# Optimization experiments

Hardware: AMD Instinct MI355X
Metric: run time of the kernel (lower is better)

The kernel has to match this reference:

```python
import jax, jax.numpy as jnp
import numpy as np

B = 65536
STATE_DIM = 96
ACTION_DIM = 32
IN_FEATURES = STATE_DIM + ACTION_DIM  # 128
HIDDEN = 256
NUM_HEADS = 200
OUT_FEATURES = 1


def setup_inputs() -> dict:
    key = jax.random.key(0)
    ks = jax.random.split(key, 9)
    state = jax.random.normal(ks[0], (B, STATE_DIM), dtype=jnp.float32)
    action = jax.random.normal(ks[1], (B, ACTION_DIM), dtype=jnp.float32)
    alphas = jax.random.uniform(ks[2], (NUM_HEADS,), dtype=jnp.float32)
    W1 = jax.random.normal(ks[3], (HIDDEN, IN_FEATURES), dtype=jnp.float32) * 0.05
    b1 = jax.random.normal(ks[4], (HIDDEN,), dtype=jnp.float32) * 0.05
    W2 = jax.random.normal(ks[5], (HIDDEN, HIDDEN), dtype=jnp.float32) * 0.05
    b2 = jax.random.normal(ks[6], (HIDDEN,), dtype=jnp.float32) * 0.05
    # stacked head params: heads[h] is Linear(256 -> out_features)
    Wh = jax.random.normal(ks[7], (NUM_HEADS, OUT_FEATURES, HIDDEN), dtype=jnp.float32) * 0.05
    bh = jax.random.normal(ks[8], (NUM_HEADS, OUT_FEATURES), dtype=jnp.float32) * 0.05
    return {"state": state, "action": action, "alphas": alphas,
            "W1": W1, "b1": b1, "W2": W2, "b2": b2, "Wh": Wh, "bh": bh}


def reference(state, action, alphas, W1, b1, W2, b2, Wh, bh):
    x = jnp.concatenate([state, action], axis=1)          # [B, 128]
    x = jax.nn.relu(x @ W1.T + b1)                         # [B, 256]
    x = jax.nn.relu(x @ W2.T + b2)                         # [B, 256]
    # sum_h alpha_h * (x @ Wh[h].T + bh[h])  ==  x @ (sum_h alpha_h Wh[h]).T + sum_h alpha_h bh[h]
    Wc = jnp.einsum('h,hod->od', alphas, Wh)               # [out, 256]
    bc = jnp.einsum('h,ho->o', alphas, bh)                 # [out]
    return x @ Wc.T + bc                                   # [B, out]
```

## Files before the change

kernel.cpp:

```cpp
#include <hip/hip_runtime.h>
#include <hip/hip_bf16.h>


#define B_TOTAL 65536
#define SDIM 96
#define ADIM 32
#define IN_F 128
#define HID 256
#define NHEADS 200
#define BM 64
#define H1_PITCH 260

typedef __bf16 bf16;
typedef __attribute__((ext_vector_type(8))) __bf16 bf16x8;
typedef __attribute__((ext_vector_type(4))) float f32x4;

__global__ void prep_kernel(const float* __restrict__ W1, const float* __restrict__ W2,
                            const float* __restrict__ alphas, const float* __restrict__ Wh,
                            const float* __restrict__ bh,
                            bf16* __restrict__ W1bf, bf16* __restrict__ W2bf,
                            float* __restrict__ Wc) {
    int tid = blockIdx.x * blockDim.x + threadIdx.x;
    if (tid < IN_F * HID) W1bf[tid] = (bf16)W1[tid];
    if (tid < HID * HID)  W2bf[tid] = (bf16)W2[tid];
    if (tid < HID) {
        float acc = 0.f;
        #pragma unroll 8
        for (int h = 0; h < NHEADS; ++h) acc += alphas[h] * Wh[h * HID + tid];
        Wc[tid] = acc;
    }
    if (tid == HID) {
        float acc = 0.f;
        for (int h = 0; h < NHEADS; ++h) acc += alphas[h] * bh[h];
        Wc[HID] = acc;
    }
}

__global__ __launch_bounds__(256, 4) void critic_kernel(
        const float* __restrict__ state, const float* __restrict__ action,
        const float* __restrict__ b1, const float* __restrict__ b2,
        const bf16* __restrict__ W1bf, const bf16* __restrict__ W2bf,
        const float* __restrict__ Wc, float* __restrict__ out) {

    __shared__ bf16 h1s[BM * H1_PITCH];
    __shared__ float sWc[HID];
    __shared__ float sPart[4][BM];

    const int tid  = threadIdx.x;
    const int wave = tid >> 6;
    const int lane = tid & 63;
    const int q    = lane >> 4;
    const int ln   = lane & 15;
    const int colw = wave * 64;
    const int row0 = blockIdx.x * BM;

    sWc[tid] = Wc[tid];

    f32x4 acc[4][4];
    #pragma unroll
    for (int mt = 0; mt < 4; ++mt)
        #pragma unroll
        for (int nt = 0; nt < 4; ++nt)
            acc[mt][nt] = (f32x4){0.f, 0.f, 0.f, 0.f};

    #pragma unroll
    for (int ks = 0; ks < 4; ++ks) {
        const int k0 = ks * 32 + q * 8;
        bf16x8 a[4], b[4];
        #pragma unroll
        for (int mt = 0; mt < 4; ++mt) {
            const size_t row = row0 + mt * 16 + ln;
            const float* src = (ks < 3) ? (state  + row * SDIM + k0)
                                        : (action + row * ADIM + q * 8);
            float4 v0 = ((const float4*)src)[0];
            float4 v1 = ((const float4*)src)[1];
            a[mt] = (bf16x8){(bf16)v0.x, (bf16)v0.y, (bf16)v0.z, (bf16)v0.w,
                             (bf16)v1.x, (bf16)v1.y, (bf16)v1.z, (bf16)v1.w};
        }
        #pragma unroll
        for (int nt = 0; nt < 4; ++nt)
            b[nt] = *(const bf16x8*)&W1bf[(size_t)(colw + nt * 16 + ln) * IN_F + k0];
        #pragma unroll
        for (int mt = 0; mt < 4; ++mt)
            #pragma unroll
            for (int nt = 0; nt < 4; ++nt)
                acc[mt][nt] = __builtin_amdgcn_mfma_f32_16x16x32_bf16(a[mt], b[nt], acc[mt][nt], 0, 0, 0);
    }

    #pragma unroll
    for (int nt = 0; nt < 4; ++nt) {
        const int n      = colw + nt * 16 + ln;
        const float bias = b1[n];
        #pragma unroll
        for (int mt = 0; mt < 4; ++mt)
            #pragma unroll
            for (int r = 0; r < 4; ++r) {
                float v = acc[mt][nt][r] + bias;
                v = v > 0.f ? v : 0.f;
                h1s[(mt * 16 + q * 4 + r) * H1_PITCH + n] = (bf16)v;
            }
    }
    __syncthreads();

    #pragma unroll
    for (int mt = 0; mt < 4; ++mt)
        #pragma unroll
        for (int nt = 0; nt < 4; ++nt)
            acc[mt][nt] = (f32x4){0.f, 0.f, 0.f, 0.f};

    #pragma unroll
    for (int ks = 0; ks < 8; ++ks) {
        const int k0 = ks * 32 + q * 8;
        bf16x8 a[4], b[4];
        #pragma unroll
        for (int mt = 0; mt < 4; ++mt)
            a[mt] = *(const bf16x8*)&h1s[(mt * 16 + ln) * H1_PITCH + k0];
        #pragma unroll
        for (int nt = 0; nt < 4; ++nt)
            b[nt] = *(const bf16x8*)&W2bf[(size_t)(colw + nt * 16 + ln) * HID + k0];
        #pragma unroll
        for (int mt = 0; mt < 4; ++mt)
            #pragma unroll
            for (int nt = 0; nt < 4; ++nt)
                acc[mt][nt] = __builtin_amdgcn_mfma_f32_16x16x32_bf16(a[mt], b[nt], acc[mt][nt], 0, 0, 0);
    }

    float partial[4][4];
    #pragma unroll
    for (int mt = 0; mt < 4; ++mt)
        #pragma unroll
        for (int r = 0; r < 4; ++r)
            partial[mt][r] = 0.f;

    #pragma unroll
    for (int nt = 0; nt < 4; ++nt) {
        const int n      = colw + nt * 16 + ln;
        const float bias = b2[n];
        const float wc   = sWc[n];
        #pragma unroll
        for (int mt = 0; mt < 4; ++mt)
            #pragma unroll
            for (int r = 0; r < 4; ++r) {
                float v = acc[mt][nt][r] + bias;
                v = v > 0.f ? v : 0.f;
                partial[mt][r] += v * wc;
            }
    }

    #pragma unroll
    for (int off = 1; off < 16; off <<= 1)
        #pragma unroll
        for (int mt = 0; mt < 4; ++mt)
            #pragma unroll
            for (int r = 0; r < 4; ++r)
                partial[mt][r] += __shfl_xor(partial[mt][r], off, 64);

    if (ln == 0) {
        #pragma unroll
        for (int mt = 0; mt < 4; ++mt)
            #pragma unroll
            for (int r = 0; r < 4; ++r)
                sPart[wave][mt * 16 + q * 4 + r] = partial[mt][r];
    }
    __syncthreads();

    if (tid < BM) {
        float v = sPart[0][tid] + sPart[1][tid] + sPart[2][tid] + sPart[3][tid] + Wc[HID];
        out[row0 + tid] = v;
    }
}

extern "C" void kernel_launch(void* const* d_in, const int* in_sizes, int n_in,
                              void* d_out, int out_size, void* d_ws, size_t ws_size,
                              hipStream_t stream) {
    const float* state  = (const float*)d_in[0];
    const float* action = (const float*)d_in[1];
    const float* alphas = (const float*)d_in[2];
    const float* W1     = (const float*)d_in[3];
    const float* b1     = (const float*)d_in[4];
    const float* W2     = (const float*)d_in[5];
    const float* b2     = (const float*)d_in[6];
    const float* Wh     = (const float*)d_in[7];
    const float* bh     = (const float*)d_in[8];
    float* out = (float*)d_out;

    bf16*  W1bf = (bf16*)d_ws;
    bf16*  W2bf = (bf16*)((char*)d_ws + 65536);
    float* Wc   = (float*)((char*)d_ws + 65536 + 131072);

    prep_kernel<<<256, 256, 0, stream>>>(W1, W2, alphas, Wh, bh, W1bf, W2bf, Wc);
    critic_kernel<<<B_TOTAL / BM, 256, 0, stream>>>(state, action, b1, b2, W1bf, W2bf, Wc, out);
}
```

Measured before the change: 136.6 us.

## Split fused critic kernel into separate layer-1 and layer-2 GEMM kernels via global h1

The fused MLP kernel is split into two launches. The first computes layer 1, stages each wave's tile through per-wave LDS and writes the bf16 hidden activations to a workspace buffer in global memory. The second reads h1 from global memory for layer 2 and applies the head reduction. This removes the block-wide LDS barrier and the large shared buffer, and the launch bounds drop to 2 blocks per SM. In exchange it adds an extra launch and a 32 MB round trip of activations through global memory.

```diff
diff --git a/kernel.cpp b/kernel.cpp
--- a/kernel.cpp
+++ b/kernel.cpp
@@ -9,7 +9,7 @@
 #define HID 256
 #define NHEADS 200
 #define BM 64
-#define H1_PITCH 260
+#define TP 68
 
 typedef __bf16 bf16;
 typedef __attribute__((ext_vector_type(8))) __bf16 bf16x8;
@@ -36,15 +36,12 @@
     }
 }
 
-__global__ __launch_bounds__(256, 4) void critic_kernel(
+__global__ __launch_bounds__(256, 2) void gemm1_kernel(
         const float* __restrict__ state, const float* __restrict__ action,
-        const float* __restrict__ b1, const float* __restrict__ b2,
-        const bf16* __restrict__ W1bf, const bf16* __restrict__ W2bf,
-        const float* __restrict__ Wc, float* __restrict__ out) {
-
-    __shared__ bf16 h1s[BM * H1_PITCH];
-    __shared__ float sWc[HID];
-    __shared__ float sPart[4][BM];
+        const float* __restrict__ b1, const bf16* __restrict__ W1bf,
+        bf16* __restrict__ h1) {
+
+    __shared__ bf16 tbuf[4][BM * TP];
 
     const int tid  = threadIdx.x;
     const int wave = tid >> 6;
@@ -53,8 +50,6 @@
     const int ln   = lane & 15;
     const int colw = wave * 64;
     const int row0 = blockIdx.x * BM;
-
-    sWc[tid] = Wc[tid];
 
     f32x4 acc[4][4];
     #pragma unroll
@@ -87,21 +82,45 @@
                 acc[mt][nt] = __builtin_amdgcn_mfma_f32_16x16x32_bf16(a[mt], b[nt], acc[mt][nt], 0, 0, 0);
     }
 
+    bf16* tl = tbuf[wave];
     #pragma unroll
     for (int nt = 0; nt < 4; ++nt) {
-        const int n      = colw + nt * 16 + ln;
-        const float bias = b1[n];
+        const float bias = b1[colw + nt * 16 + ln];
         #pragma unroll
         for (int mt = 0; mt < 4; ++mt)
             #pragma unroll
             for (int r = 0; r < 4; ++r) {
                 float v = acc[mt][nt][r] + bias;
                 v = v > 0.f ? v : 0.f;
-                h1s[(mt * 16 + q * 4 + r) * H1_PITCH + n] = (bf16)v;
+                tl[(mt * 16 + q * 4 + r) * TP + nt * 16 + ln] = (bf16)v;
             }
     }
-    __syncthreads();
-
+    const int r8 = lane >> 3;
+    const int c8 = lane & 7;
+    #pragma unroll
+    for (int i = 0; i < 8; ++i) {
+        const int row = i * 8 + r8;
+        bf16x8 v = *(const bf16x8*)&tl[row * TP + c8 * 8];
+        *(bf16x8*)&h1[(size_t)(row0 + row) * HID + colw + c8 * 8] = v;
+    }
+}
+
+__global__ __launch_bounds__(256, 2) void gemm2_kernel(
+        const bf16* __restrict__ h1, const float* __restrict__ b2,
+        const bf16* __restrict__ W2bf, const float* __restrict__ Wc,
+        float* __restrict__ out) {
+
+    __shared__ float sPart[4][BM];
+
+    const int tid  = threadIdx.x;
+    const int wave = tid >> 6;
+    const int lane = tid & 63;
+    const int q    = lane >> 4;
+    const int ln   = lane & 15;
+    const int colw = wave * 64;
+    const int row0 = blockIdx.x * BM;
+
+    f32x4 acc[4][4];
     #pragma unroll
     for (int mt = 0; mt < 4; ++mt)
         #pragma unroll
@@ -114,7 +133,7 @@
         bf16x8 a[4], b[4];
         #pragma unroll
         for (int mt = 0; mt < 4; ++mt)
-            a[mt] = *(const bf16x8*)&h1s[(mt * 16 + ln) * H1_PITCH + k0];
+            a[mt] = *(const bf16x8*)&h1[(size_t)(row0 + mt * 16 + ln) * HID + k0];
         #pragma unroll
         for (int nt = 0; nt < 4; ++nt)
             b[nt] = *(const bf16x8*)&W2bf[(size_t)(colw + nt * 16 + ln) * HID + k0];
@@ -134,9 +153,9 @@
 
     #pragma unroll
     for (int nt = 0; nt < 4; ++nt) {
-        const int n      = colw + nt * 16 + ln;
+        const int n = colw + nt * 16 + ln;
         const float bias = b2[n];
-        const float wc   = sWc[n];
+        const float wc   = Wc[n];
         #pragma unroll
         for (int mt = 0; mt < 4; ++mt)
             #pragma unroll
@@ -187,7 +206,9 @@
     bf16*  W1bf = (bf16*)d_ws;
     bf16*  W2bf = (bf16*)((char*)d_ws + 65536);
     float* Wc   = (float*)((char*)d_ws + 65536 + 131072);
+    bf16*  h1   = (bf16*)((char*)d_ws + 262144);
 
     prep_kernel<<<256, 256, 0, stream>>>(W1, W2, alphas, Wh, bh, W1bf, W2bf, Wc);
-    critic_kernel<<<B_TOTAL / BM, 256, 0, stream>>>(state, action, b1, b2, W1bf, W2bf, Wc, out);
-}
+    gemm1_kernel<<<B_TOTAL / BM, 256, 0, stream>>>(state, action, b1, W1bf, h1);
+    gemm2_kernel<<<B_TOTAL / BM, 256, 0, stream>>>(h1, b2, W2bf, Wc, out);
+}
```

Result: slower. 153.7 us (+12.5%).
